# Kernel optimization log

Measured on AMD Instinct MI355X. Metric: run time of the kernel, lower is better.

## Reference

```python
import jax, jax.numpy as jnp
import numpy as np

B, T, V, F = 32, 128, 128, 64
K_ORDER = 3
N_FILT = 64

def setup_inputs() -> dict:
    key = jax.random.key(0)
    k1, k2, k3 = jax.random.split(key, 3)
    x = jax.random.normal(k1, (B, T, V, F), dtype=jnp.float32)
    W = jax.random.uniform(k2, (B, V, V), dtype=jnp.float32)  # learned adjacency, nonneg
    # keras 'uniform' initializer default range [-0.05, 0.05]
    Theta = jax.random.uniform(k3, (K_ORDER, F, N_FILT), dtype=jnp.float32, minval=-0.05, maxval=0.05)
    return {"x": x, "W": W, "Theta": Theta}

def reference(x, W, Theta):
    # x: (B,T,V,F), W: (B,V,V), Theta: (k,F,O)
    k = Theta.shape[0]
    v = x.shape[2]
    eye = jnp.eye(v, dtype=x.dtype)
    deg = jnp.sum(W, axis=1)                      # (B,V) -- sum over axis=1 as in K.sum(W, axis=1)
    D = eye[None, :, :] * deg[:, :, None]         # matrix_diag(deg)
    L = D - W
    L_t = L - eye[None, :, :]                     # 2*L/lambda_max - I with lambda_max=2
    chebs = [jnp.broadcast_to(eye[None, :, :], W.shape), L_t]
    for i in range(2, k):
        # NOTE: elementwise multiply, faithful to the original tf code (tf `*`)
        chebs.append(2.0 * L_t * chebs[-1] - chebs[-2])
    Tk = jnp.stack(chebs, axis=0)                 # (k,B,V,V)
    # out[b,t,u,o] = sum_{k,v,f} Tk[k,b,v,u] * x[b,t,v,f] * Theta[k,f,o]
    # (T_k transposed matmul graph_signal, then dot with theta_k, summed over k and t-batched)
    out = jnp.einsum('kbvu,btvf,kfo->btuo', Tk, x, Theta)
    return jax.nn.relu(out)
```

## Files before the change

### kernel.cpp

```cpp
#include <hip/hip_runtime.h>

typedef __attribute__((ext_vector_type(8))) short bf16x8;
typedef __attribute__((ext_vector_type(4))) float f32x4;

namespace {

constexpr int B = 32, T = 128, V = 128, F = 64, O = 64;
constexpr int TPB = 16;

constexpr size_t WS_THT_OFF = (size_t)B * 64 * 64 * 8 * 2;
constexpr size_t WS_LDG_OFF = WS_THT_OFF + 1536 * 8 * 2;

__device__ inline unsigned short f2bf(float f) {
    unsigned u = __builtin_bit_cast(unsigned, f);
    u += 0x7FFFu + ((u >> 16) & 1u);
    return (unsigned short)(u >> 16);
}

__global__ __launch_bounds__(256) void prep(const float* __restrict__ W,
                                            const float* __restrict__ Theta,
                                            unsigned short* __restrict__ acat_f,
                                            unsigned short* __restrict__ tht_f,
                                            float* __restrict__ ldg) {
    const int tid = threadIdx.x;
    if (blockIdx.x == B) {
        for (int i = 0; i < 6; ++i) {
            int fi = tid + i * 256;
            int ks = fi / 768, rem = fi % 768;
            int nf = rem >> 6, lane = rem & 63;
            int n = nf * 16 + (lane & 15);
            int f0 = ks * 32 + (lane >> 4) * 8;
            unsigned short vals[8];
#pragma unroll
            for (int j = 0; j < 8; ++j) {
                int f = f0 + j;
                float v;
                if (n < 64)       v = Theta[f * 64 + n] - Theta[2 * 4096 + f * 64 + n];
                else if (n < 128) v = Theta[4096 + f * 64 + (n - 64)];
                else              v = Theta[2 * 4096 + f * 64 + (n - 128)];
                vals[j] = f2bf(v);
            }
            *(bf16x8*)(tht_f + (size_t)fi * 8) = *(bf16x8*)vals;
        }
        return;
    }
    const int b = blockIdx.x;
    const float* Wb = W + (size_t)b * V * V;
    __shared__ float Wl[V][V + 1];
    for (int i = 0; i < V * V / 256; ++i) {
        int idx = tid + i * 256;
        Wl[idx >> 7][idx & 127] = Wb[idx];
    }
    __syncthreads();
    if (tid < V) {
        float s = 0.f;
        for (int i = 0; i < V; ++i) s += Wl[i][tid];
        ldg[b * V + tid] = s - 1.0f - Wl[tid][tid];
    }
    unsigned short* ab_f = acat_f + (size_t)b * 32768;
    for (int i = 0; i < 16; ++i) {
        int fi = tid + i * 256;
        int ks = fi >> 9, rem = fi & 511;
        int r2 = rem >> 6, lane = rem & 63;
        int u = r2 * 16 + (lane & 15);
        int kv0 = ks * 32 + (lane >> 4) * 8;
        unsigned short vals[8];
#pragma unroll
        for (int j = 0; j < 8; ++j) {
            int kv = kv0 + j, v = kv & 127;
            float wv = Wl[v][u];
            float val = (v == u) ? 0.f : ((kv < 128) ? -wv : 2.f * wv * wv);
            vals[j] = f2bf(val);
        }
        *(bf16x8*)(ab_f + (size_t)fi * 8) = *(bf16x8*)vals;
    }
}

__global__ __launch_bounds__(512, 1) void graph_conv_main(
    const float* __restrict__ x, const unsigned short* __restrict__ acat_f,
    const unsigned short* __restrict__ tht_f, const float* __restrict__ ldg,
    float* __restrict__ out) {
    const int t0 = blockIdx.x * TPB, b = blockIdx.y;
    const int tid = threadIdx.x;
    const int lane = tid & 63, w = tid >> 6;
    const int uq = w & 3;
    const int oh = w >> 2;
    const int lr = lane & 15, lg = lane >> 4;

    __shared__ __align__(16) unsigned short tht_s[12288];
    __shared__ __align__(16) unsigned short acat_s[32768];
    __shared__ __align__(16) unsigned short xbuf[2][8192];
    __shared__ __align__(16) unsigned short zc[16384];

    const float* xb = x + ((size_t)(b * T + t0)) * (V * F);

    f32x4 ldv[2], ld2v[2];
#pragma unroll
    for (int uf = 0; uf < 2; ++uf) {
        ldv[uf] = *(const f32x4*)(ldg + b * V + 32 * uq + 16 * uf + lg * 4);
        ld2v[uf] = 2.0f * ldv[uf] * ldv[uf];
    }

    {
        const unsigned short* ag = acat_f + (size_t)b * 32768;
#pragma unroll
        for (int i = 0; i < 8; ++i) {
            int c = tid + i * 512;
            __builtin_amdgcn_global_load_lds(
                (const __attribute__((address_space(1))) void*)(ag + c * 8),
                (__attribute__((address_space(3))) void*)(acat_s + c * 8), 16, 0, 0);
        }
#pragma unroll
        for (int i = 0; i < 3; ++i) {
            int c = tid + i * 512;
            __builtin_amdgcn_global_load_lds(
                (const __attribute__((address_space(1))) void*)(tht_f + c * 8),
                (__attribute__((address_space(3))) void*)(tht_s + c * 8), 16, 0, 0);
        }
    }

    auto load_pf = [&](int tt, float4 (&pf)[4]) {
        const float4* src = (const float4*)(xb + (size_t)tt * (V * F));
#pragma unroll
        for (int i = 0; i < 4; ++i) pf[i] = src[tid + i * 512];
    };
    auto store_pf = [&](int buf, float4 (&pf)[4]) {
#pragma unroll
        for (int i = 0; i < 4; ++i) {
            int p = tid + i * 512;
            int row = p >> 4, c4 = p & 15;
            uint2 q;
            q.x = f2bf(pf[i].x) | ((unsigned)f2bf(pf[i].y) << 16);
            q.y = f2bf(pf[i].z) | ((unsigned)f2bf(pf[i].w) << 16);
            *(uint2*)((char*)xbuf[buf] +
                      row * 128 + (((c4 >> 1) ^ (row & 7)) << 4) + (c4 & 1) * 8) = q;
        }
    };

    float4 pfA[4], pfB[4];
    load_pf(0, pfA);
    load_pf(1, pfB);
    asm volatile("s_waitcnt vmcnt(0)" ::: "memory");
    __builtin_amdgcn_sched_barrier(0);
    store_pf(0, pfA);
    asm volatile("s_waitcnt lgkmcnt(0)" ::: "memory");
    __builtin_amdgcn_sched_barrier(0);
    __builtin_amdgcn_s_barrier();
    __builtin_amdgcn_sched_barrier(0);

    auto iter = [&](int tt, float4 (&pfRdy)[4], float4 (&pfNew)[4]) {
        const int cur = tt & 1;
        if (tt + 2 < TPB) load_pf(tt + 2, pfNew);

        bf16x8 xa[2][2];
#pragma unroll
        for (int rv = 0; rv < 2; ++rv) {
            const int row = 32 * uq + 16 * rv + lr;
            const char* rp = (const char*)xbuf[cur] + row * 128;
            const int rs = row & 7;
#pragma unroll
            for (int kf = 0; kf < 2; ++kf)
                xa[rv][kf] = *(const bf16x8*)(rp + (((kf * 4 + lg) ^ rs) << 4));
        }

        f32x4 acc[2][2], z1[2][2], z2[2][2];
#pragma unroll
        for (int a = 0; a < 2; ++a)
#pragma unroll
            for (int o = 0; o < 2; ++o) {
                acc[a][o] = (f32x4){0.f, 0.f, 0.f, 0.f};
                z1[a][o] = (f32x4){0.f, 0.f, 0.f, 0.f};
                z2[a][o] = (f32x4){0.f, 0.f, 0.f, 0.f};
            }
#pragma unroll
        for (int kf = 0; kf < 2; ++kf)
#pragma unroll
            for (int i = 0; i < 2; ++i) {
                bf16x8 t0b = *(const bf16x8*)(tht_s + ((kf * 12 + 0 + 2 * oh + i) * 64 + lane) * 8);
                bf16x8 t1b = *(const bf16x8*)(tht_s + ((kf * 12 + 4 + 2 * oh + i) * 64 + lane) * 8);
                bf16x8 t2b = *(const bf16x8*)(tht_s + ((kf * 12 + 8 + 2 * oh + i) * 64 + lane) * 8);
#pragma unroll
                for (int rv = 0; rv < 2; ++rv) {
                    acc[rv][i] = __builtin_amdgcn_mfma_f32_16x16x32_bf16(xa[rv][kf], t0b, acc[rv][i], 0, 0, 0);
                    z1[rv][i] = __builtin_amdgcn_mfma_f32_16x16x32_bf16(xa[rv][kf], t1b, z1[rv][i], 0, 0, 0);
                    z2[rv][i] = __builtin_amdgcn_mfma_f32_16x16x32_bf16(xa[rv][kf], t2b, z2[rv][i], 0, 0, 0);
                }
            }

        char* zc1p = (char*)zc;
        char* zc2p = (char*)zc + 16384;
#pragma unroll
        for (int uf = 0; uf < 2; ++uf)
#pragma unroll
            for (int of = 0; of < 2; ++of) {
                acc[uf][of] += ldv[uf] * z1[uf][of] + ld2v[uf] * z2[uf][of];
                const int ro = 32 * oh + of * 16 + lr;
                const int slot = 4 * uq + 2 * uf + (lg >> 1);
                const int byte = ro * 256 + (((slot ^ lr)) << 4) + (lg & 1) * 8;
                f32x4 v1 = z1[uf][of], v2 = z2[uf][of];
                uint2 q1, q2;
                q1.x = f2bf(v1[0]) | ((unsigned)f2bf(v1[1]) << 16);
                q1.y = f2bf(v1[2]) | ((unsigned)f2bf(v1[3]) << 16);
                q2.x = f2bf(v2[0]) | ((unsigned)f2bf(v2[1]) << 16);
                q2.y = f2bf(v2[2]) | ((unsigned)f2bf(v2[3]) << 16);
                *(uint2*)(zc1p + byte) = q1;
                *(uint2*)(zc2p + byte) = q2;
            }

        asm volatile("s_waitcnt lgkmcnt(0)" ::: "memory");
        __builtin_amdgcn_sched_barrier(0);
        __builtin_amdgcn_s_barrier();
        __builtin_amdgcn_sched_barrier(0);

#pragma unroll
        for (int kk = 0; kk < 8; ++kk) {
            const char* zsrc = (kk < 4) ? zc1p : zc2p;
            bf16x8 af[2];
#pragma unroll
            for (int uf = 0; uf < 2; ++uf)
                af[uf] = *(const bf16x8*)(acat_s + ((kk * 8 + 2 * uq + uf) * 64 + lane) * 8);
            bf16x8 zb[2];
#pragma unroll
            for (int of = 0; of < 2; ++of) {
                const int ro = 32 * oh + of * 16 + lr;
                const int slot = (kk & 3) * 4 + lg;
                zb[of] = *(const bf16x8*)(zsrc + ro * 256 + ((slot ^ lr) << 4));
            }
#pragma unroll
            for (int uf = 0; uf < 2; ++uf)
#pragma unroll
                for (int of = 0; of < 2; ++of)
                    acc[uf][of] = __builtin_amdgcn_mfma_f32_16x16x32_bf16(af[uf], zb[of], acc[uf][of], 0, 0, 0);
        }

        if (tt + 1 < TPB) {
            if (tt + 2 < TPB) {
                asm volatile("s_waitcnt vmcnt(4)" ::: "memory");
            } else {
                asm volatile("s_waitcnt vmcnt(0)" ::: "memory");
            }
            __builtin_amdgcn_sched_barrier(0);
            store_pf(cur ^ 1, pfRdy);
        }

        asm volatile("s_waitcnt lgkmcnt(0)" ::: "memory");
        __builtin_amdgcn_sched_barrier(0);
        __builtin_amdgcn_s_barrier();
        __builtin_amdgcn_sched_barrier(0);

        float* os = (float*)zc;
#pragma unroll
        for (int uf = 0; uf < 2; ++uf)
#pragma unroll
            for (int of = 0; of < 2; ++of)
#pragma unroll
                for (int j = 0; j < 4; ++j) {
                    const int u = 32 * uq + 16 * uf + lg * 4 + j;
                    const int o = 32 * oh + 16 * of + lr;
                    const float r = acc[uf][of][j];
                    os[u * 64 + o] = r > 0.f ? r : 0.f;
                }

        asm volatile("s_waitcnt lgkmcnt(0)" ::: "memory");
        __builtin_amdgcn_sched_barrier(0);
        __builtin_amdgcn_s_barrier();
        __builtin_amdgcn_sched_barrier(0);

        {
            float* obt = out + ((size_t)(b * T + t0 + tt)) * (V * O);
            const float4* osv = (const float4*)zc;
#pragma unroll
            for (int i = 0; i < 4; ++i) {
                const int idx = tid + i * 512;
                *(float4*)(obt + idx * 4) = osv[idx];
            }
        }

        asm volatile("s_waitcnt lgkmcnt(0)" ::: "memory");
        __builtin_amdgcn_sched_barrier(0);
        __builtin_amdgcn_s_barrier();
        __builtin_amdgcn_sched_barrier(0);
    };

    for (int tt = 0; tt < TPB; tt += 2) {
        iter(tt, pfB, pfA);
        iter(tt + 1, pfA, pfB);
    }
}

}

extern "C" void kernel_launch(void* const* d_in, const int* in_sizes, int n_in,
                              void* d_out, int out_size, void* d_ws, size_t ws_size,
                              hipStream_t stream) {
    const float* x = (const float*)d_in[0];
    const float* W = (const float*)d_in[1];
    const float* Theta = (const float*)d_in[2];
    float* outp = (float*)d_out;

    unsigned short* acat_f = (unsigned short*)d_ws;
    unsigned short* tht_f = (unsigned short*)((char*)d_ws + WS_THT_OFF);
    float* ldg = (float*)((char*)d_ws + WS_LDG_OFF);

    prep<<<B + 1, 256, 0, stream>>>(W, Theta, acat_f, tht_f, ldg);
    graph_conv_main<<<dim3(T / TPB, B), 512, 0, stream>>>(x, acat_f, tht_f, ldg, outp);
}
```

Measured before the change: 79.22 us.

## Compute transposed accumulator so results store directly to global, dropping LDS staging

Computes the output accumulator in transposed orientation (swapping MFMA operands) so each lane holds four consecutive output channels and can write float4 straight to global memory. This removes the LDS round-trip for the output tile and two block barriers per timestep. In exchange it issues extra MFMAs, recomputing the x·Theta products in transposed form (z1T, z2T, accT) alongside the normal z1/z2 still needed for the LDS B-operand, which raises MFMA count and register pressure.

```diff
diff --git a/kernel.cpp b/kernel.cpp
--- a/kernel.cpp
+++ b/kernel.cpp
@@ -94,11 +94,11 @@
 
     const float* xb = x + ((size_t)(b * T + t0)) * (V * F);
 
-    f32x4 ldv[2], ld2v[2];
+    float lds_s[2], ld2_s[2];
 #pragma unroll
     for (int uf = 0; uf < 2; ++uf) {
-        ldv[uf] = *(const f32x4*)(ldg + b * V + 32 * uq + 16 * uf + lg * 4);
-        ld2v[uf] = 2.0f * ldv[uf] * ldv[uf];
+        lds_s[uf] = ldg[b * V + 32 * uq + 16 * uf + lr];
+        ld2_s[uf] = 2.0f * lds_s[uf] * lds_s[uf];
     }
 
     {
@@ -163,12 +163,14 @@
                 xa[rv][kf] = *(const bf16x8*)(rp + (((kf * 4 + lg) ^ rs) << 4));
         }
 
-        f32x4 acc[2][2], z1[2][2], z2[2][2];
+        f32x4 accT[2][2], z1T[2][2], z2T[2][2], z1[2][2], z2[2][2];
 #pragma unroll
         for (int a = 0; a < 2; ++a)
 #pragma unroll
             for (int o = 0; o < 2; ++o) {
-                acc[a][o] = (f32x4){0.f, 0.f, 0.f, 0.f};
+                accT[a][o] = (f32x4){0.f, 0.f, 0.f, 0.f};
+                z1T[a][o] = (f32x4){0.f, 0.f, 0.f, 0.f};
+                z2T[a][o] = (f32x4){0.f, 0.f, 0.f, 0.f};
                 z1[a][o] = (f32x4){0.f, 0.f, 0.f, 0.f};
                 z2[a][o] = (f32x4){0.f, 0.f, 0.f, 0.f};
             }
@@ -181,11 +183,19 @@
                 bf16x8 t2b = *(const bf16x8*)(tht_s + ((kf * 12 + 8 + 2 * oh + i) * 64 + lane) * 8);
 #pragma unroll
                 for (int rv = 0; rv < 2; ++rv) {
-                    acc[rv][i] = __builtin_amdgcn_mfma_f32_16x16x32_bf16(xa[rv][kf], t0b, acc[rv][i], 0, 0, 0);
-                    z1[rv][i] = __builtin_amdgcn_mfma_f32_16x16x32_bf16(xa[rv][kf], t1b, z1[rv][i], 0, 0, 0);
-                    z2[rv][i] = __builtin_amdgcn_mfma_f32_16x16x32_bf16(xa[rv][kf], t2b, z2[rv][i], 0, 0, 0);
+                    z1[rv][i]  = __builtin_amdgcn_mfma_f32_16x16x32_bf16(xa[rv][kf], t1b, z1[rv][i], 0, 0, 0);
+                    z2[rv][i]  = __builtin_amdgcn_mfma_f32_16x16x32_bf16(xa[rv][kf], t2b, z2[rv][i], 0, 0, 0);
+                    accT[i][rv] = __builtin_amdgcn_mfma_f32_16x16x32_bf16(t0b, xa[rv][kf], accT[i][rv], 0, 0, 0);
+                    z1T[i][rv] = __builtin_amdgcn_mfma_f32_16x16x32_bf16(t1b, xa[rv][kf], z1T[i][rv], 0, 0, 0);
+                    z2T[i][rv] = __builtin_amdgcn_mfma_f32_16x16x32_bf16(t2b, xa[rv][kf], z2T[i][rv], 0, 0, 0);
                 }
             }
+
+#pragma unroll
+        for (int of = 0; of < 2; ++of)
+#pragma unroll
+            for (int uf = 0; uf < 2; ++uf)
+                accT[of][uf] += lds_s[uf] * z1T[of][uf] + ld2_s[uf] * z2T[of][uf];
 
         char* zc1p = (char*)zc;
         char* zc2p = (char*)zc + 16384;
@@ -193,7 +203,6 @@
         for (int uf = 0; uf < 2; ++uf)
 #pragma unroll
             for (int of = 0; of < 2; ++of) {
-                acc[uf][of] += ldv[uf] * z1[uf][of] + ld2v[uf] * z2[uf][of];
                 const int ro = 32 * oh + of * 16 + lr;
                 const int slot = 4 * uq + 2 * uf + (lg >> 1);
                 const int byte = ro * 256 + (((slot ^ lr)) << 4) + (lg & 1) * 8;
@@ -227,10 +236,10 @@
                 zb[of] = *(const bf16x8*)(zsrc + ro * 256 + ((slot ^ lr) << 4));
             }
 #pragma unroll
-            for (int uf = 0; uf < 2; ++uf)
-#pragma unroll
-                for (int of = 0; of < 2; ++of)
-                    acc[uf][of] = __builtin_amdgcn_mfma_f32_16x16x32_bf16(af[uf], zb[of], acc[uf][of], 0, 0, 0);
+            for (int of = 0; of < 2; ++of)
+#pragma unroll
+                for (int uf = 0; uf < 2; ++uf)
+                    accT[of][uf] = __builtin_amdgcn_mfma_f32_16x16x32_bf16(zb[of], af[uf], accT[of][uf], 0, 0, 0);
         }
 
         if (tt + 1 < TPB) {
@@ -243,37 +252,19 @@
             store_pf(cur ^ 1, pfRdy);
         }
 
-        asm volatile("s_waitcnt lgkmcnt(0)" ::: "memory");
-        __builtin_amdgcn_sched_barrier(0);
-        __builtin_amdgcn_s_barrier();
-        __builtin_amdgcn_sched_barrier(0);
-
-        float* os = (float*)zc;
-#pragma unroll
-        for (int uf = 0; uf < 2; ++uf)
-#pragma unroll
-            for (int of = 0; of < 2; ++of)
-#pragma unroll
-                for (int j = 0; j < 4; ++j) {
-                    const int u = 32 * uq + 16 * uf + lg * 4 + j;
-                    const int o = 32 * oh + 16 * of + lr;
-                    const float r = acc[uf][of][j];
-                    os[u * 64 + o] = r > 0.f ? r : 0.f;
-                }
-
-        asm volatile("s_waitcnt lgkmcnt(0)" ::: "memory");
-        __builtin_amdgcn_sched_barrier(0);
-        __builtin_amdgcn_s_barrier();
-        __builtin_amdgcn_sched_barrier(0);
-
         {
             float* obt = out + ((size_t)(b * T + t0 + tt)) * (V * O);
-            const float4* osv = (const float4*)zc;
-#pragma unroll
-            for (int i = 0; i < 4; ++i) {
-                const int idx = tid + i * 512;
-                *(float4*)(obt + idx * 4) = osv[idx];
-            }
+#pragma unroll
+            for (int of = 0; of < 2; ++of)
+#pragma unroll
+                for (int uf = 0; uf < 2; ++uf) {
+                    const int u = 32 * uq + 16 * uf + lr;
+                    const int o = 32 * oh + 16 * of + lg * 4;
+                    f32x4 r = accT[of][uf];
+#pragma unroll
+                    for (int j = 0; j < 4; ++j) r[j] = r[j] > 0.f ? r[j] : 0.f;
+                    *(f32x4*)(obt + u * 64 + o) = r;
+                }
         }
 
         asm volatile("s_waitcnt lgkmcnt(0)" ::: "memory");
```

Result: slower. 88.30 us (+11.5%).

## Process two timesteps per iteration and read adjacency fragments from global

Applied to the files above, without the earlier changes.

Restructures the main loop to handle two timesteps per iteration. This doubles the LDS buffers for x and the intermediate z, and halves the number of barriers per timestep. The adjacency A fragments are no longer staged into LDS; they are loaded straight from global memory (L2-cached) and each load is reused across both timesteps. The change trades LDS capacity for more accumulator registers and in-flight prefetch registers. It risks register pressure and global-load latency in the second matmul stage.

```diff
diff --git a/kernel.cpp b/kernel.cpp
--- a/kernel.cpp
+++ b/kernel.cpp
@@ -88,11 +88,11 @@
     const int lr = lane & 15, lg = lane >> 4;
 
     __shared__ __align__(16) unsigned short tht_s[12288];
-    __shared__ __align__(16) unsigned short acat_s[32768];
-    __shared__ __align__(16) unsigned short xbuf[2][8192];
-    __shared__ __align__(16) unsigned short zc[16384];
+    __shared__ __align__(16) unsigned short xbuf[2][2][8192];
+    __shared__ __align__(16) unsigned short zc[2][16384];
 
     const float* xb = x + ((size_t)(b * T + t0)) * (V * F);
+    const unsigned short* ag = acat_f + (size_t)b * 32768;
 
     f32x4 ldv[2], ld2v[2];
 #pragma unroll
@@ -101,77 +101,74 @@
         ld2v[uf] = 2.0f * ldv[uf] * ldv[uf];
     }
 
-    {
-        const unsigned short* ag = acat_f + (size_t)b * 32768;
+#pragma unroll
+    for (int i = 0; i < 3; ++i) {
+        int c = tid + i * 512;
+        __builtin_amdgcn_global_load_lds(
+            (const __attribute__((address_space(1))) void*)(tht_f + c * 8),
+            (__attribute__((address_space(3))) void*)(tht_s + c * 8), 16, 0, 0);
+    }
+
+    float4 pf[8];
+    auto load_pf = [&](int pr) {
+        const float4* s0 = (const float4*)(xb + (size_t)(2 * pr) * (V * F));
+        const float4* s1 = (const float4*)(xb + (size_t)(2 * pr + 1) * (V * F));
+#pragma unroll
+        for (int i = 0; i < 4; ++i) pf[i] = s0[tid + i * 512];
+#pragma unroll
+        for (int i = 0; i < 4; ++i) pf[4 + i] = s1[tid + i * 512];
+    };
+    auto store_pf = [&](int buf) {
 #pragma unroll
         for (int i = 0; i < 8; ++i) {
-            int c = tid + i * 512;
-            __builtin_amdgcn_global_load_lds(
-                (const __attribute__((address_space(1))) void*)(ag + c * 8),
-                (__attribute__((address_space(3))) void*)(acat_s + c * 8), 16, 0, 0);
-        }
-#pragma unroll
-        for (int i = 0; i < 3; ++i) {
-            int c = tid + i * 512;
-            __builtin_amdgcn_global_load_lds(
-                (const __attribute__((address_space(1))) void*)(tht_f + c * 8),
-                (__attribute__((address_space(3))) void*)(tht_s + c * 8), 16, 0, 0);
-        }
-    }
-
-    auto load_pf = [&](int tt, float4 (&pf)[4]) {
-        const float4* src = (const float4*)(xb + (size_t)tt * (V * F));
-#pragma unroll
-        for (int i = 0; i < 4; ++i) pf[i] = src[tid + i * 512];
-    };
-    auto store_pf = [&](int buf, float4 (&pf)[4]) {
-#pragma unroll
-        for (int i = 0; i < 4; ++i) {
-            int p = tid + i * 512;
+            int tp = i >> 2;
+            int p = tid + (i & 3) * 512;
             int row = p >> 4, c4 = p & 15;
             uint2 q;
             q.x = f2bf(pf[i].x) | ((unsigned)f2bf(pf[i].y) << 16);
             q.y = f2bf(pf[i].z) | ((unsigned)f2bf(pf[i].w) << 16);
-            *(uint2*)((char*)xbuf[buf] +
+            *(uint2*)((char*)xbuf[buf][tp] +
                       row * 128 + (((c4 >> 1) ^ (row & 7)) << 4) + (c4 & 1) * 8) = q;
         }
     };
 
-    float4 pfA[4], pfB[4];
-    load_pf(0, pfA);
-    load_pf(1, pfB);
+    load_pf(0);
     asm volatile("s_waitcnt vmcnt(0)" ::: "memory");
     __builtin_amdgcn_sched_barrier(0);
-    store_pf(0, pfA);
+    store_pf(0);
     asm volatile("s_waitcnt lgkmcnt(0)" ::: "memory");
     __builtin_amdgcn_sched_barrier(0);
     __builtin_amdgcn_s_barrier();
     __builtin_amdgcn_sched_barrier(0);
 
-    auto iter = [&](int tt, float4 (&pfRdy)[4], float4 (&pfNew)[4]) {
-        const int cur = tt & 1;
-        if (tt + 2 < TPB) load_pf(tt + 2, pfNew);
-
-        bf16x8 xa[2][2];
-#pragma unroll
-        for (int rv = 0; rv < 2; ++rv) {
-            const int row = 32 * uq + 16 * rv + lr;
-            const char* rp = (const char*)xbuf[cur] + row * 128;
-            const int rs = row & 7;
-#pragma unroll
-            for (int kf = 0; kf < 2; ++kf)
-                xa[rv][kf] = *(const bf16x8*)(rp + (((kf * 4 + lg) ^ rs) << 4));
-        }
-
-        f32x4 acc[2][2], z1[2][2], z2[2][2];
-#pragma unroll
-        for (int a = 0; a < 2; ++a)
-#pragma unroll
-            for (int o = 0; o < 2; ++o) {
-                acc[a][o] = (f32x4){0.f, 0.f, 0.f, 0.f};
-                z1[a][o] = (f32x4){0.f, 0.f, 0.f, 0.f};
-                z2[a][o] = (f32x4){0.f, 0.f, 0.f, 0.f};
-            }
+    for (int si = 0; si < TPB / 2; ++si) {
+        const int cur = si & 1;
+        if (si + 1 < TPB / 2) load_pf(si + 1);
+
+        bf16x8 xa[2][2][2];
+#pragma unroll
+        for (int tp = 0; tp < 2; ++tp)
+#pragma unroll
+            for (int rv = 0; rv < 2; ++rv) {
+                const int row = 32 * uq + 16 * rv + lr;
+                const char* rp = (const char*)xbuf[cur][tp] + row * 128;
+                const int rs = row & 7;
+#pragma unroll
+                for (int kf = 0; kf < 2; ++kf)
+                    xa[tp][rv][kf] = *(const bf16x8*)(rp + (((kf * 4 + lg) ^ rs) << 4));
+            }
+
+        f32x4 acc[2][2][2], z1[2][2][2], z2[2][2][2];
+#pragma unroll
+        for (int tp = 0; tp < 2; ++tp)
+#pragma unroll
+            for (int a = 0; a < 2; ++a)
+#pragma unroll
+                for (int o = 0; o < 2; ++o) {
+                    acc[tp][a][o] = (f32x4){0.f, 0.f, 0.f, 0.f};
+                    z1[tp][a][o] = (f32x4){0.f, 0.f, 0.f, 0.f};
+                    z2[tp][a][o] = (f32x4){0.f, 0.f, 0.f, 0.f};
+                }
 #pragma unroll
         for (int kf = 0; kf < 2; ++kf)
 #pragma unroll
@@ -180,32 +177,37 @@
                 bf16x8 t1b = *(const bf16x8*)(tht_s + ((kf * 12 + 4 + 2 * oh + i) * 64 + lane) * 8);
                 bf16x8 t2b = *(const bf16x8*)(tht_s + ((kf * 12 + 8 + 2 * oh + i) * 64 + lane) * 8);
 #pragma unroll
-                for (int rv = 0; rv < 2; ++rv) {
-                    acc[rv][i] = __builtin_amdgcn_mfma_f32_16x16x32_bf16(xa[rv][kf], t0b, acc[rv][i], 0, 0, 0);
-                    z1[rv][i] = __builtin_amdgcn_mfma_f32_16x16x32_bf16(xa[rv][kf], t1b, z1[rv][i], 0, 0, 0);
-                    z2[rv][i] = __builtin_amdgcn_mfma_f32_16x16x32_bf16(xa[rv][kf], t2b, z2[rv][i], 0, 0, 0);
+                for (int tp = 0; tp < 2; ++tp)
+#pragma unroll
+                    for (int rv = 0; rv < 2; ++rv) {
+                        acc[tp][rv][i] = __builtin_amdgcn_mfma_f32_16x16x32_bf16(xa[tp][rv][kf], t0b, acc[tp][rv][i], 0, 0, 0);
+                        z1[tp][rv][i]  = __builtin_amdgcn_mfma_f32_16x16x32_bf16(xa[tp][rv][kf], t1b, z1[tp][rv][i], 0, 0, 0);
+                        z2[tp][rv][i]  = __builtin_amdgcn_mfma_f32_16x16x32_bf16(xa[tp][rv][kf], t2b, z2[tp][rv][i], 0, 0, 0);
+                    }
+            }
+
+#pragma unroll
+        for (int tp = 0; tp < 2; ++tp) {
+            char* zc1p = (char*)zc[tp];
+            char* zc2p = (char*)zc[tp] + 16384;
+#pragma unroll
+            for (int uf = 0; uf < 2; ++uf)
+#pragma unroll
+                for (int of = 0; of < 2; ++of) {
+                    acc[tp][uf][of] += ldv[uf] * z1[tp][uf][of] + ld2v[uf] * z2[tp][uf][of];
+                    const int ro = 32 * oh + of * 16 + lr;
+                    const int slot = 4 * uq + 2 * uf + (lg >> 1);
+                    const int byte = ro * 256 + (((slot ^ lr)) << 4) + (lg & 1) * 8;
+                    f32x4 v1 = z1[tp][uf][of], v2 = z2[tp][uf][of];
+                    uint2 q1, q2;
+                    q1.x = f2bf(v1[0]) | ((unsigned)f2bf(v1[1]) << 16);
+                    q1.y = f2bf(v1[2]) | ((unsigned)f2bf(v1[3]) << 16);
+                    q2.x = f2bf(v2[0]) | ((unsigned)f2bf(v2[1]) << 16);
+                    q2.y = f2bf(v2[2]) | ((unsigned)f2bf(v2[3]) << 16);
+                    *(uint2*)(zc1p + byte) = q1;
+                    *(uint2*)(zc2p + byte) = q2;
                 }
-            }
-
-        char* zc1p = (char*)zc;
-        char* zc2p = (char*)zc + 16384;
-#pragma unroll
-        for (int uf = 0; uf < 2; ++uf)
-#pragma unroll
-            for (int of = 0; of < 2; ++of) {
-                acc[uf][of] += ldv[uf] * z1[uf][of] + ld2v[uf] * z2[uf][of];
-                const int ro = 32 * oh + of * 16 + lr;
-                const int slot = 4 * uq + 2 * uf + (lg >> 1);
-                const int byte = ro * 256 + (((slot ^ lr)) << 4) + (lg & 1) * 8;
-                f32x4 v1 = z1[uf][of], v2 = z2[uf][of];
-                uint2 q1, q2;
-                q1.x = f2bf(v1[0]) | ((unsigned)f2bf(v1[1]) << 16);
-                q1.y = f2bf(v1[2]) | ((unsigned)f2bf(v1[3]) << 16);
-                q2.x = f2bf(v2[0]) | ((unsigned)f2bf(v2[1]) << 16);
-                q2.y = f2bf(v2[2]) | ((unsigned)f2bf(v2[3]) << 16);
-                *(uint2*)(zc1p + byte) = q1;
-                *(uint2*)(zc2p + byte) = q2;
-            }
+        }
 
         asm volatile("s_waitcnt lgkmcnt(0)" ::: "memory");
         __builtin_amdgcn_sched_barrier(0);
@@ -214,33 +216,49 @@
 
 #pragma unroll
         for (int kk = 0; kk < 8; ++kk) {
-            const char* zsrc = (kk < 4) ? zc1p : zc2p;
             bf16x8 af[2];
 #pragma unroll
             for (int uf = 0; uf < 2; ++uf)
-                af[uf] = *(const bf16x8*)(acat_s + ((kk * 8 + 2 * uq + uf) * 64 + lane) * 8);
-            bf16x8 zb[2];
-#pragma unroll
-            for (int of = 0; of < 2; ++of) {
-                const int ro = 32 * oh + of * 16 + lr;
-                const int slot = (kk & 3) * 4 + lg;
-                zb[of] = *(const bf16x8*)(zsrc + ro * 256 + ((slot ^ lr) << 4));
-            }
+                af[uf] = *(const bf16x8*)(ag + ((kk * 8 + 2 * uq + uf) * 64 + lane) * 8);
+#pragma unroll
+            for (int tp = 0; tp < 2; ++tp) {
+                const char* zsrc = (char*)zc[tp] + (kk < 4 ? 0 : 16384);
+                bf16x8 zb[2];
+#pragma unroll
+                for (int of = 0; of < 2; ++of) {
+                    const int ro = 32 * oh + of * 16 + lr;
+                    const int slot = (kk & 3) * 4 + lg;
+                    zb[of] = *(const bf16x8*)(zsrc + ro * 256 + ((slot ^ lr) << 4));
+                }
+#pragma unroll
+                for (int uf = 0; uf < 2; ++uf)
+#pragma unroll
+                    for (int of = 0; of < 2; ++of)
+                        acc[tp][uf][of] = __builtin_amdgcn_mfma_f32_16x16x32_bf16(af[uf], zb[of], acc[tp][uf][of], 0, 0, 0);
+            }
+        }
+
+        if (si + 1 < TPB / 2) store_pf(cur ^ 1);
+
+        asm volatile("s_waitcnt lgkmcnt(0)" ::: "memory");
+        __builtin_amdgcn_sched_barrier(0);
+        __builtin_amdgcn_s_barrier();
+        __builtin_amdgcn_sched_barrier(0);
+
+#pragma unroll
+        for (int tp = 0; tp < 2; ++tp) {
+            float* os = (float*)&zc[0][0] + tp * 8192;
 #pragma unroll
             for (int uf = 0; uf < 2; ++uf)
 #pragma unroll
                 for (int of = 0; of < 2; ++of)
-                    acc[uf][of] = __builtin_amdgcn_mfma_f32_16x16x32_bf16(af[uf], zb[of], acc[uf][of], 0, 0, 0);
-        }
-
-        if (tt + 1 < TPB) {
-            if (tt + 2 < TPB) {
-                asm volatile("s_waitcnt vmcnt(4)" ::: "memory");
-            } else {
-                asm volatile("s_waitcnt vmcnt(0)" ::: "memory");
-            }
-            __builtin_amdgcn_sched_barrier(0);
-            store_pf(cur ^ 1, pfRdy);
+#pragma unroll
+                    for (int j = 0; j < 4; ++j) {
+                        const int u = 32 * uq + 16 * uf + lg * 4 + j;
+                        const int o = 32 * oh + 16 * of + lr;
+                        const float r = acc[tp][uf][of][j];
+                        os[u * 64 + o] = r > 0.f ? r : 0.f;
+                    }
         }
 
         asm volatile("s_waitcnt lgkmcnt(0)" ::: "memory");
@@ -248,27 +266,10 @@
         __builtin_amdgcn_s_barrier();
         __builtin_amdgcn_sched_barrier(0);
 
-        float* os = (float*)zc;
-#pragma unroll
-        for (int uf = 0; uf < 2; ++uf)
-#pragma unroll
-            for (int of = 0; of < 2; ++of)
-#pragma unroll
-                for (int j = 0; j < 4; ++j) {
-                    const int u = 32 * uq + 16 * uf + lg * 4 + j;
-                    const int o = 32 * oh + 16 * of + lr;
-                    const float r = acc[uf][of][j];
-                    os[u * 64 + o] = r > 0.f ? r : 0.f;
-                }
-
-        asm volatile("s_waitcnt lgkmcnt(0)" ::: "memory");
-        __builtin_amdgcn_sched_barrier(0);
-        __builtin_amdgcn_s_barrier();
-        __builtin_amdgcn_sched_barrier(0);
-
-        {
-            float* obt = out + ((size_t)(b * T + t0 + tt)) * (V * O);
-            const float4* osv = (const float4*)zc;
+#pragma unroll
+        for (int tp = 0; tp < 2; ++tp) {
+            float* obt = out + ((size_t)(b * T + t0 + 2 * si + tp)) * (V * O);
+            const float4* osv = (const float4*)((float*)&zc[0][0] + tp * 8192);
 #pragma unroll
             for (int i = 0; i < 4; ++i) {
                 const int idx = tid + i * 512;
@@ -280,11 +281,6 @@
         __builtin_amdgcn_sched_barrier(0);
         __builtin_amdgcn_s_barrier();
         __builtin_amdgcn_sched_barrier(0);
-    };
-
-    for (int tt = 0; tt < TPB; tt += 2) {
-        iter(tt, pfB, pfA);
-        iter(tt + 1, pfA, pfB);
     }
 }
 
```

Result: slower. 136.4 us (+72.2%).
